# Kernel tuning notes

Measured on AMD Instinct MI355X. Metric: run time of the kernel, lower is better.

## Reference

```python
import jax, jax.numpy as jnp
import numpy as np

D_MODEL = 1024
NUM_HEADS = 16
D_K = D_MODEL // NUM_HEADS


def setup_inputs() -> dict:
    key = jax.random.key(0)
    ks = jax.random.split(key, 11)
    B, S = 4, 2048
    scale = 1.0 / np.sqrt(D_MODEL)
    inp = {
        'query': jax.random.normal(ks[0], (B, S, D_MODEL), jnp.float32),
        'key': jax.random.normal(ks[1], (B, S, D_MODEL), jnp.float32),
        'value': jax.random.normal(ks[2], (B, S, D_MODEL), jnp.float32),
        'Wq': jax.random.normal(ks[3], (D_MODEL, D_MODEL), jnp.float32) * scale,
        'bq': jnp.zeros((D_MODEL,), jnp.float32),
        'Wk': jax.random.normal(ks[4], (D_MODEL, D_MODEL), jnp.float32) * scale,
        'bk': jnp.zeros((D_MODEL,), jnp.float32),
        'Wv': jax.random.normal(ks[5], (D_MODEL, D_MODEL), jnp.float32) * scale,
        'bv': jnp.zeros((D_MODEL,), jnp.float32),
        'Wo': jax.random.normal(ks[6], (D_MODEL, D_MODEL), jnp.float32) * scale,
        'bo': jnp.zeros((D_MODEL,), jnp.float32),
    }
    return inp


def _split_heads(x):
    # [B, S, D] -> [B, H, S, d_k]
    B, S, _ = x.shape
    return x.reshape(B, S, NUM_HEADS, D_K).transpose(0, 2, 1, 3)


def reference(query, key, value, Wq, bq, Wk, bk, Wv, bv, Wo, bo):
    # torch nn.Linear: y = x @ W.T + b
    q = _split_heads(query @ Wq.T + bq)   # [B,H,Sq,dk]
    k = _split_heads(key @ Wk.T + bk)     # [B,H,Sk,dk]
    v = _split_heads(value @ Wv.T + bv)   # [B,H,Sk,dk]
    scores = jnp.einsum('bhqd,bhkd->bhqk', q, k) / jnp.sqrt(jnp.float32(D_K))
    attn = jax.nn.softmax(scores, axis=-1)
    out = jnp.einsum('bhqk,bhkd->bhqd', attn, v)  # [B,H,Sq,dk]
    B, H, Sq, dk = out.shape
    out = out.transpose(0, 2, 1, 3).reshape(B, Sq, D_MODEL)
    return out @ Wo.T + bo
```

## Files before the change

### kernel.cpp

```cpp
#include <hip/hip_runtime.h>

typedef short bf16x8 __attribute__((ext_vector_type(8)));
typedef float f32x4 __attribute__((ext_vector_type(4)));
typedef unsigned short u16;

#define S_LEN 2048
#define DM 1024
#define NH 16
#define DK 64
#define BHD ((size_t)S_LEN * DK)

#define QSCALE 0.18033688011112042f

static __device__ __forceinline__ u16 f2bf(float f) {
  union { float f; unsigned u; } x; x.f = f;
  unsigned r = x.u + 0x7FFFu + ((x.u >> 16) & 1u);
  return (u16)(r >> 16);
}

static __device__ __forceinline__ void gload_lds16(const u16* g, u16* l) {
  __builtin_amdgcn_global_load_lds(
      (const __attribute__((address_space(1))) unsigned int*)g,
      (__attribute__((address_space(3))) unsigned int*)l, 16, 0, 0);
}

__global__ __launch_bounds__(256) void conv_all(
    const float* __restrict__ q, const float* __restrict__ k, const float* __restrict__ v,
    const float* __restrict__ Wq, const float* __restrict__ Wk,
    const float* __restrict__ Wv, const float* __restrict__ Wo,
    u16* __restrict__ xq, u16* __restrict__ xk, u16* __restrict__ xv,
    u16* __restrict__ wb) {
  const int b = blockIdx.x;
  const float* s; u16* d; float sc = 1.0f; int i;
  if (b < 8192) {
    s = q; d = xq; sc = QSCALE; i = b * 256 + threadIdx.x;
  } else if (b < 16384) {
    s = k; d = xk; i = (b - 8192) * 256 + threadIdx.x;
  } else if (b < 24576) {
    s = v; d = xv; i = (b - 16384) * 256 + threadIdx.x;
  } else {
    int b2 = b - 24576, wsel = b2 >> 10;
    s = (wsel == 0) ? Wq : (wsel == 1) ? Wk : (wsel == 2) ? Wv : Wo;
    d = wb + (size_t)wsel * 1048576;
    i = (b2 & 1023) * 256 + threadIdx.x;
  }
  float4 vv = ((const float4*)s)[i];
  ushort4 h;
  h.x = f2bf(vv.x * sc); h.y = f2bf(vv.y * sc);
  h.z = f2bf(vv.z * sc); h.w = f2bf(vv.w * sc);
  ((ushort4*)d)[i] = h;
}

#define GSTAGE(DST, SRC)                                                          \
  {                                                                               \
    _Pragma("unroll") for (int j = 0; j < 4; ++j) {                               \
      gload_lds16((SRC) + (size_t)(j * 32 + (w << 3) + (l >> 3)) * 1024 +         \
                      (size_t)(((l & 7) ^ (l >> 3)) * 8),                         \
                  (DST) + (j * 256 + w * 64) * 8);                                \
    }                                                                             \
  }

__global__ __launch_bounds__(256) void proj_gemm(
    const u16* __restrict__ xq, const u16* __restrict__ xk, const u16* __restrict__ xv,
    const u16* __restrict__ wb,
    const float* __restrict__ bq, const float* __restrict__ bk, const float* __restrict__ bv,
    u16* __restrict__ qws, u16* __restrict__ kws, u16* __restrict__ vws)
{
  __shared__ u16 Al[128 * 64];
  __shared__ u16 Bl[128 * 64];
  const int z = blockIdx.z;
  const u16* Xb = (z == 0) ? xq : (z == 1) ? xk : xv;
  const u16* Wb = wb + (size_t)z * 1048576;
  const float* bias = (z == 0) ? bq : (z == 1) ? bk : bv;
  const float bscale = (z == 0) ? QSCALE : 1.0f;

  const int t = threadIdx.x;
  const int l = t & 63, w = t >> 6;
  const int lr = l & 15, lg = l >> 4;
  const int wm = w >> 1, wn = w & 1;
  const int m0 = blockIdx.x * 128, n0 = blockIdx.y * 128;
  const int sxr = lr & 7;

  f32x4 acc[4][4] = {};
  for (int k0 = 0; k0 < DM; k0 += 64) {
    __syncthreads();
    GSTAGE(Al, Xb + (size_t)m0 * 1024 + k0)
    GSTAGE(Bl, Wb + (size_t)n0 * 1024 + k0)
    __syncthreads();

    bf16x8 a[4][2], b[4][2];
#pragma unroll
    for (int mi = 0; mi < 4; ++mi) {
      const u16* rp = Al + (wm * 64 + mi * 16 + lr) * 64;
      a[mi][0] = *(const bf16x8*)(rp + ((lg ^ sxr) * 8));
      a[mi][1] = *(const bf16x8*)(rp + (((4 + lg) ^ sxr) * 8));
    }
#pragma unroll
    for (int ni = 0; ni < 4; ++ni) {
      const u16* rp = Bl + (wn * 64 + ni * 16 + lr) * 64;
      b[ni][0] = *(const bf16x8*)(rp + ((lg ^ sxr) * 8));
      b[ni][1] = *(const bf16x8*)(rp + (((4 + lg) ^ sxr) * 8));
    }
    __builtin_amdgcn_s_setprio(1);
#pragma unroll
    for (int mi = 0; mi < 4; ++mi)
#pragma unroll
      for (int ni = 0; ni < 4; ++ni) {
        acc[mi][ni] = __builtin_amdgcn_mfma_f32_16x16x32_bf16(a[mi][0], b[ni][0], acc[mi][ni], 0, 0, 0);
        acc[mi][ni] = __builtin_amdgcn_mfma_f32_16x16x32_bf16(a[mi][1], b[ni][1], acc[mi][ni], 0, 0, 0);
      }
    __builtin_amdgcn_s_setprio(0);
  }

#pragma unroll
  for (int mi = 0; mi < 4; ++mi) {
#pragma unroll
    for (int ni = 0; ni < 4; ++ni) {
#pragma unroll
      for (int r = 0; r < 4; ++r) {
        int m = m0 + wm * 64 + mi * 16 + lg * 4 + r;
        int n = n0 + wn * 64 + ni * 16 + lr;
        float y = acc[mi][ni][r] + bias[n] * bscale;
        u16 h = f2bf(y);
        int b_ = m >> 11, s = m & 2047, hh = n >> 6, d = n & 63;
        size_t head = (size_t)(b_ * NH + hh);
        if (z == 0)      qws[head * BHD + (size_t)s * DK + d] = h;
        else if (z == 1) kws[head * BHD + (size_t)s * DK + d] = h;
        else             vws[head * BHD + (size_t)d * S_LEN + s] = h;
      }
    }
  }
}

__global__ __launch_bounds__(256) void oproj_gemm(
    const u16* __restrict__ Ab, const u16* __restrict__ Wob,
    const float* __restrict__ bo, float* __restrict__ out)
{
  __shared__ u16 Al[128 * 64];
  __shared__ u16 Bl[128 * 64];
  const int t = threadIdx.x;
  const int l = t & 63, w = t >> 6;
  const int lr = l & 15, lg = l >> 4;
  const int wm = w >> 1, wn = w & 1;
  const int m0 = blockIdx.x * 128, n0 = blockIdx.y * 128;
  const int sxr = lr & 7;

  f32x4 acc[4][4] = {};
  for (int k0 = 0; k0 < DM; k0 += 64) {
    __syncthreads();
    GSTAGE(Al, Ab + (size_t)m0 * 1024 + k0)
    GSTAGE(Bl, Wob + (size_t)n0 * 1024 + k0)
    __syncthreads();

    bf16x8 a[4][2], b[4][2];
#pragma unroll
    for (int mi = 0; mi < 4; ++mi) {
      const u16* rp = Al + (wm * 64 + mi * 16 + lr) * 64;
      a[mi][0] = *(const bf16x8*)(rp + ((lg ^ sxr) * 8));
      a[mi][1] = *(const bf16x8*)(rp + (((4 + lg) ^ sxr) * 8));
    }
#pragma unroll
    for (int ni = 0; ni < 4; ++ni) {
      const u16* rp = Bl + (wn * 64 + ni * 16 + lr) * 64;
      b[ni][0] = *(const bf16x8*)(rp + ((lg ^ sxr) * 8));
      b[ni][1] = *(const bf16x8*)(rp + (((4 + lg) ^ sxr) * 8));
    }
    __builtin_amdgcn_s_setprio(1);
#pragma unroll
    for (int mi = 0; mi < 4; ++mi)
#pragma unroll
      for (int ni = 0; ni < 4; ++ni) {
        acc[mi][ni] = __builtin_amdgcn_mfma_f32_16x16x32_bf16(a[mi][0], b[ni][0], acc[mi][ni], 0, 0, 0);
        acc[mi][ni] = __builtin_amdgcn_mfma_f32_16x16x32_bf16(a[mi][1], b[ni][1], acc[mi][ni], 0, 0, 0);
      }
    __builtin_amdgcn_s_setprio(0);
  }

#pragma unroll
  for (int mi = 0; mi < 4; ++mi) {
#pragma unroll
    for (int ni = 0; ni < 4; ++ni) {
#pragma unroll
      for (int r = 0; r < 4; ++r) {
        int m = m0 + wm * 64 + mi * 16 + lg * 4 + r;
        int n = n0 + wn * 64 + ni * 16 + lr;
        out[(size_t)m * DM + n] = acc[mi][ni][r] + bo[n];
      }
    }
  }
}

__global__ __launch_bounds__(512, 8) void attn_kernel(
    const u16* __restrict__ qh, const u16* __restrict__ kh,
    const u16* __restrict__ vt, u16* __restrict__ aout)
{
  __shared__ u16 KT[2][64 * 64];
  __shared__ u16 VT[2][64 * 64];

  const int t = threadIdx.x;
  const int l = t & 63, w = t >> 6;
  const int lr = l & 15, lg = l >> 4;

  const int bid = blockIdx.x;
  const int logical = (bid & 7) * 128 + (bid >> 3);
  const int bh = logical >> 4;
  const int qb = (logical & 15) * 128 + w * 16;

  const u16* qp = qh + (size_t)bh * BHD;
  const u16* kp = kh + (size_t)bh * BHD;
  const u16* vp = vt + (size_t)bh * BHD;
  const int sx = lr & 7;

  const int srow = t >> 3;
  const int scolS = (t & 7) ^ (srow & 7);

  bf16x8 qf[2];
#pragma unroll
  for (int c = 0; c < 2; ++c)
    qf[c] = *(const bf16x8*)(qp + (size_t)(qb + lr) * DK + c * 32 + lg * 8);

  f32x4 acc[4] = {};
  float lsum = 0.0f;

#define STAGE(B, KV)                                                           \
  {                                                                            \
    gload_lds16(kp + (size_t)((KV) + srow) * DK + scolS * 8, &KT[B][w * 512]); \
    gload_lds16(vp + (size_t)srow * S_LEN + (KV) + scolS * 8, &VT[B][w * 512]);\
  }

  STAGE(0, 0)

  for (int i = 0; i < 32; ++i) {
    __syncthreads();
    if (i < 31) STAGE((i + 1) & 1, (i + 1) * 64)

    const u16* Kb = &KT[i & 1][0];
    const u16* Vb = &VT[i & 1][0];

    f32x4 sc[4] = {};
    __builtin_amdgcn_s_setprio(1);
#pragma unroll
    for (int ct = 0; ct < 4; ++ct) {
      bf16x8 k0 = *(const bf16x8*)(Kb + (ct * 16 + lr) * 64 + ((lg ^ sx) * 8));
      bf16x8 k1 = *(const bf16x8*)(Kb + (ct * 16 + lr) * 64 + (((4 + lg) ^ sx) * 8));
      sc[ct] = __builtin_amdgcn_mfma_f32_16x16x32_bf16(k0, qf[0], sc[ct], 0, 0, 0);
      sc[ct] = __builtin_amdgcn_mfma_f32_16x16x32_bf16(k1, qf[1], sc[ct], 0, 0, 0);
    }
    __builtin_amdgcn_s_setprio(0);

    unsigned cpk[4][2];
    float psum = 0.0f;
#pragma unroll
    for (int ct = 0; ct < 4; ++ct) {
      float p0 = __builtin_amdgcn_exp2f(sc[ct][0] - 8.0f);
      float p1 = __builtin_amdgcn_exp2f(sc[ct][1] - 8.0f);
      float p2 = __builtin_amdgcn_exp2f(sc[ct][2] - 8.0f);
      float p3 = __builtin_amdgcn_exp2f(sc[ct][3] - 8.0f);
      psum += (p0 + p1) + (p2 + p3);
      asm("v_cvt_pk_bf16_f32 %0, %1, %2" : "=v"(cpk[ct][0]) : "v"(p0), "v"(p1));
      asm("v_cvt_pk_bf16_f32 %0, %1, %2" : "=v"(cpk[ct][1]) : "v"(p2), "v"(p3));
    }
    lsum += psum;

    bf16x8 pf[2];
#pragma unroll
    for (int kk = 0; kk < 2; ++kk) {
      unsigned a0 = cpk[2 * kk][0], b0 = cpk[2 * kk + 1][0];
      unsigned a1 = cpk[2 * kk][1], b1 = cpk[2 * kk + 1][1];
      asm("v_permlane32_swap_b32 %0, %1" : "+v"(a0), "+v"(b0));
      asm("v_permlane16_swap_b32 %0, %1" : "+v"(a0), "+v"(b0));
      asm("v_permlane32_swap_b32 %0, %1" : "+v"(a1), "+v"(b1));
      asm("v_permlane16_swap_b32 %0, %1" : "+v"(a1), "+v"(b1));
      union { unsigned u[4]; bf16x8 v; } tmp;
      tmp.u[0] = a0; tmp.u[1] = a1; tmp.u[2] = b0; tmp.u[3] = b1;
      pf[kk] = tmp.v;
    }

    __builtin_amdgcn_s_setprio(1);
#pragma unroll
    for (int ni = 0; ni < 4; ++ni) {
      bf16x8 vf0 = *(const bf16x8*)(Vb + (ni * 16 + lr) * 64 + ((lg ^ sx) * 8));
      bf16x8 vf1 = *(const bf16x8*)(Vb + (ni * 16 + lr) * 64 + (((4 + lg) ^ sx) * 8));
      acc[ni] = __builtin_amdgcn_mfma_f32_16x16x32_bf16(pf[0], vf0, acc[ni], 0, 0, 0);
      acc[ni] = __builtin_amdgcn_mfma_f32_16x16x32_bf16(pf[1], vf1, acc[ni], 0, 0, 0);
    }
    __builtin_amdgcn_s_setprio(0);
  }
#undef STAGE

  const int b_ = bh >> 4, hh = bh & 15;
  float s_ = lsum;
  s_ += __shfl_xor(s_, 16);
  s_ += __shfl_xor(s_, 32);
  float inv = 1.0f / s_;
  float iv[4];
  iv[0] = __shfl(inv, lg * 4 + 0);
  iv[1] = __shfl(inv, lg * 4 + 1);
  iv[2] = __shfl(inv, lg * 4 + 2);
  iv[3] = __shfl(inv, lg * 4 + 3);
#pragma unroll
  for (int r = 0; r < 4; ++r) {
    int s = qb + lg * 4 + r;
#pragma unroll
    for (int ni = 0; ni < 4; ++ni)
      aout[((size_t)(b_ * S_LEN + s)) * DM + hh * DK + ni * 16 + lr] =
          f2bf(acc[ni][r] * iv[r]);
  }
}

extern "C" void kernel_launch(void* const* d_in, const int* in_sizes, int n_in,
                              void* d_out, int out_size, void* d_ws, size_t ws_size,
                              hipStream_t stream) {
  (void)in_sizes; (void)n_in; (void)out_size; (void)ws_size;
  const float* q  = (const float*)d_in[0];
  const float* k  = (const float*)d_in[1];
  const float* v  = (const float*)d_in[2];
  const float* Wq = (const float*)d_in[3];
  const float* bq = (const float*)d_in[4];
  const float* Wk = (const float*)d_in[5];
  const float* bk = (const float*)d_in[6];
  const float* Wv = (const float*)d_in[7];
  const float* bv = (const float*)d_in[8];
  const float* Wo = (const float*)d_in[9];
  const float* bo = (const float*)d_in[10];
  float* out = (float*)d_out;

  u16* qws = (u16*)d_ws;
  u16* kws = qws + (size_t)8388608;
  u16* vws = kws + (size_t)8388608;
  u16* xb  = vws + (size_t)8388608;
  u16* wb  = xb  + (size_t)8388608;
  u16* aws = xb;
  u16* kxb = (u16*)d_out;
  u16* vxb = kxb + (size_t)8388608;

  conv_all<<<dim3(28672), dim3(256), 0, stream>>>(q, k, v, Wq, Wk, Wv, Wo, xb, kxb, vxb, wb);

  proj_gemm<<<dim3(64, 8, 3), dim3(256), 0, stream>>>(xb, kxb, vxb, wb, bq, bk, bv,
                                                      qws, kws, vws);

  attn_kernel<<<dim3(1024), dim3(512), 0, stream>>>(qws, kws, vws, aws);

  oproj_gemm<<<dim3(64, 8), dim3(256), 0, stream>>>(aws, wb + 3145728, bo, out);
}
```

Baseline: 213.5 us.

## Process two 16-row query tiles per wave in attention to reuse K/V fragments

Each wave in the attention kernel now handles 32 query rows, as two 16-row MFMA tiles, instead of 16. Each K and V fragment read from LDS therefore feeds twice as many MFMAs, and each block covers 256 query rows, so the grid is halved. This cuts LDS reads and global K/V staging per unit of work. The cost is more registers per wave (launch bounds drop from 8 to 4 blocks) and half as many blocks for latency hiding.

Result: no change. 211.0 us (-1.2%).

```diff
diff --git a/kernel.cpp b/kernel.cpp
--- a/kernel.cpp
+++ b/kernel.cpp
@@ -190,7 +190,7 @@
   }
 }
 
-__global__ __launch_bounds__(512, 8) void attn_kernel(
+__global__ __launch_bounds__(512, 4) void attn_kernel(
     const u16* __restrict__ qh, const u16* __restrict__ kh,
     const u16* __restrict__ vt, u16* __restrict__ aout)
 {
@@ -202,9 +202,9 @@
   const int lr = l & 15, lg = l >> 4;
 
   const int bid = blockIdx.x;
-  const int logical = (bid & 7) * 128 + (bid >> 3);
-  const int bh = logical >> 4;
-  const int qb = (logical & 15) * 128 + w * 16;
+  const int logical = (bid & 7) * 64 + (bid >> 3);
+  const int bh = logical >> 3;
+  const int qb = (logical & 7) * 256 + w * 32;
 
   const u16* qp = qh + (size_t)bh * BHD;
   const u16* kp = kh + (size_t)bh * BHD;
@@ -214,13 +214,15 @@
   const int srow = t >> 3;
   const int scolS = (t & 7) ^ (srow & 7);
 
-  bf16x8 qf[2];
-#pragma unroll
-  for (int c = 0; c < 2; ++c)
-    qf[c] = *(const bf16x8*)(qp + (size_t)(qb + lr) * DK + c * 32 + lg * 8);
-
-  f32x4 acc[4] = {};
-  float lsum = 0.0f;
+  bf16x8 qf[2][2];
+#pragma unroll
+  for (int qi = 0; qi < 2; ++qi)
+#pragma unroll
+    for (int c = 0; c < 2; ++c)
+      qf[qi][c] = *(const bf16x8*)(qp + (size_t)(qb + qi * 16 + lr) * DK + c * 32 + lg * 8);
+
+  f32x4 acc[4][2] = {};
+  float lsum[2] = { 0.0f, 0.0f };
 
 #define STAGE(B, KV)                                                           \
   {                                                                            \
@@ -237,74 +239,86 @@
     const u16* Kb = &KT[i & 1][0];
     const u16* Vb = &VT[i & 1][0];
 
-    f32x4 sc[4] = {};
+    f32x4 sc[4][2] = {};
     __builtin_amdgcn_s_setprio(1);
 #pragma unroll
     for (int ct = 0; ct < 4; ++ct) {
       bf16x8 k0 = *(const bf16x8*)(Kb + (ct * 16 + lr) * 64 + ((lg ^ sx) * 8));
       bf16x8 k1 = *(const bf16x8*)(Kb + (ct * 16 + lr) * 64 + (((4 + lg) ^ sx) * 8));
-      sc[ct] = __builtin_amdgcn_mfma_f32_16x16x32_bf16(k0, qf[0], sc[ct], 0, 0, 0);
-      sc[ct] = __builtin_amdgcn_mfma_f32_16x16x32_bf16(k1, qf[1], sc[ct], 0, 0, 0);
+      sc[ct][0] = __builtin_amdgcn_mfma_f32_16x16x32_bf16(k0, qf[0][0], sc[ct][0], 0, 0, 0);
+      sc[ct][0] = __builtin_amdgcn_mfma_f32_16x16x32_bf16(k1, qf[0][1], sc[ct][0], 0, 0, 0);
+      sc[ct][1] = __builtin_amdgcn_mfma_f32_16x16x32_bf16(k0, qf[1][0], sc[ct][1], 0, 0, 0);
+      sc[ct][1] = __builtin_amdgcn_mfma_f32_16x16x32_bf16(k1, qf[1][1], sc[ct][1], 0, 0, 0);
     }
     __builtin_amdgcn_s_setprio(0);
 
-    unsigned cpk[4][2];
-    float psum = 0.0f;
-#pragma unroll
-    for (int ct = 0; ct < 4; ++ct) {
-      float p0 = __builtin_amdgcn_exp2f(sc[ct][0] - 8.0f);
-      float p1 = __builtin_amdgcn_exp2f(sc[ct][1] - 8.0f);
-      float p2 = __builtin_amdgcn_exp2f(sc[ct][2] - 8.0f);
-      float p3 = __builtin_amdgcn_exp2f(sc[ct][3] - 8.0f);
-      psum += (p0 + p1) + (p2 + p3);
-      asm("v_cvt_pk_bf16_f32 %0, %1, %2" : "=v"(cpk[ct][0]) : "v"(p0), "v"(p1));
-      asm("v_cvt_pk_bf16_f32 %0, %1, %2" : "=v"(cpk[ct][1]) : "v"(p2), "v"(p3));
-    }
-    lsum += psum;
-
-    bf16x8 pf[2];
-#pragma unroll
-    for (int kk = 0; kk < 2; ++kk) {
-      unsigned a0 = cpk[2 * kk][0], b0 = cpk[2 * kk + 1][0];
-      unsigned a1 = cpk[2 * kk][1], b1 = cpk[2 * kk + 1][1];
-      asm("v_permlane32_swap_b32 %0, %1" : "+v"(a0), "+v"(b0));
-      asm("v_permlane16_swap_b32 %0, %1" : "+v"(a0), "+v"(b0));
-      asm("v_permlane32_swap_b32 %0, %1" : "+v"(a1), "+v"(b1));
-      asm("v_permlane16_swap_b32 %0, %1" : "+v"(a1), "+v"(b1));
-      union { unsigned u[4]; bf16x8 v; } tmp;
-      tmp.u[0] = a0; tmp.u[1] = a1; tmp.u[2] = b0; tmp.u[3] = b1;
-      pf[kk] = tmp.v;
-    }
+    unsigned cpk[2][4][2];
+#pragma unroll
+    for (int qi = 0; qi < 2; ++qi) {
+      float psum = 0.0f;
+#pragma unroll
+      for (int ct = 0; ct < 4; ++ct) {
+        float p0 = __builtin_amdgcn_exp2f(sc[ct][qi][0] - 8.0f);
+        float p1 = __builtin_amdgcn_exp2f(sc[ct][qi][1] - 8.0f);
+        float p2 = __builtin_amdgcn_exp2f(sc[ct][qi][2] - 8.0f);
+        float p3 = __builtin_amdgcn_exp2f(sc[ct][qi][3] - 8.0f);
+        psum += (p0 + p1) + (p2 + p3);
+        asm("v_cvt_pk_bf16_f32 %0, %1, %2" : "=v"(cpk[qi][ct][0]) : "v"(p0), "v"(p1));
+        asm("v_cvt_pk_bf16_f32 %0, %1, %2" : "=v"(cpk[qi][ct][1]) : "v"(p2), "v"(p3));
+      }
+      lsum[qi] += psum;
+    }
+
+    bf16x8 pf[2][2];
+#pragma unroll
+    for (int qi = 0; qi < 2; ++qi)
+#pragma unroll
+      for (int kk = 0; kk < 2; ++kk) {
+        unsigned a0 = cpk[qi][2 * kk][0], b0 = cpk[qi][2 * kk + 1][0];
+        unsigned a1 = cpk[qi][2 * kk][1], b1 = cpk[qi][2 * kk + 1][1];
+        asm("v_permlane32_swap_b32 %0, %1" : "+v"(a0), "+v"(b0));
+        asm("v_permlane16_swap_b32 %0, %1" : "+v"(a0), "+v"(b0));
+        asm("v_permlane32_swap_b32 %0, %1" : "+v"(a1), "+v"(b1));
+        asm("v_permlane16_swap_b32 %0, %1" : "+v"(a1), "+v"(b1));
+        union { unsigned u[4]; bf16x8 v; } tmp;
+        tmp.u[0] = a0; tmp.u[1] = a1; tmp.u[2] = b0; tmp.u[3] = b1;
+        pf[qi][kk] = tmp.v;
+      }
 
     __builtin_amdgcn_s_setprio(1);
 #pragma unroll
     for (int ni = 0; ni < 4; ++ni) {
       bf16x8 vf0 = *(const bf16x8*)(Vb + (ni * 16 + lr) * 64 + ((lg ^ sx) * 8));
       bf16x8 vf1 = *(const bf16x8*)(Vb + (ni * 16 + lr) * 64 + (((4 + lg) ^ sx) * 8));
-      acc[ni] = __builtin_amdgcn_mfma_f32_16x16x32_bf16(pf[0], vf0, acc[ni], 0, 0, 0);
-      acc[ni] = __builtin_amdgcn_mfma_f32_16x16x32_bf16(pf[1], vf1, acc[ni], 0, 0, 0);
+      acc[ni][0] = __builtin_amdgcn_mfma_f32_16x16x32_bf16(pf[0][0], vf0, acc[ni][0], 0, 0, 0);
+      acc[ni][0] = __builtin_amdgcn_mfma_f32_16x16x32_bf16(pf[0][1], vf1, acc[ni][0], 0, 0, 0);
+      acc[ni][1] = __builtin_amdgcn_mfma_f32_16x16x32_bf16(pf[1][0], vf0, acc[ni][1], 0, 0, 0);
+      acc[ni][1] = __builtin_amdgcn_mfma_f32_16x16x32_bf16(pf[1][1], vf1, acc[ni][1], 0, 0, 0);
     }
     __builtin_amdgcn_s_setprio(0);
   }
 #undef STAGE
 
   const int b_ = bh >> 4, hh = bh & 15;
-  float s_ = lsum;
-  s_ += __shfl_xor(s_, 16);
-  s_ += __shfl_xor(s_, 32);
-  float inv = 1.0f / s_;
-  float iv[4];
-  iv[0] = __shfl(inv, lg * 4 + 0);
-  iv[1] = __shfl(inv, lg * 4 + 1);
-  iv[2] = __shfl(inv, lg * 4 + 2);
-  iv[3] = __shfl(inv, lg * 4 + 3);
-#pragma unroll
-  for (int r = 0; r < 4; ++r) {
-    int s = qb + lg * 4 + r;
-#pragma unroll
-    for (int ni = 0; ni < 4; ++ni)
-      aout[((size_t)(b_ * S_LEN + s)) * DM + hh * DK + ni * 16 + lr] =
-          f2bf(acc[ni][r] * iv[r]);
+#pragma unroll
+  for (int qi = 0; qi < 2; ++qi) {
+    float s_ = lsum[qi];
+    s_ += __shfl_xor(s_, 16);
+    s_ += __shfl_xor(s_, 32);
+    float inv = 1.0f / s_;
+    float iv[4];
+    iv[0] = __shfl(inv, lg * 4 + 0);
+    iv[1] = __shfl(inv, lg * 4 + 1);
+    iv[2] = __shfl(inv, lg * 4 + 2);
+    iv[3] = __shfl(inv, lg * 4 + 3);
+#pragma unroll
+    for (int r = 0; r < 4; ++r) {
+      int s = qb + qi * 16 + lg * 4 + r;
+#pragma unroll
+      for (int ni = 0; ni < 4; ++ni)
+        aout[((size_t)(b_ * S_LEN + s)) * DM + hh * DK + ni * 16 + lr] =
+            f2bf(acc[ni][qi][r] * iv[r]);
+    }
   }
 }
 
@@ -339,7 +353,7 @@
   proj_gemm<<<dim3(64, 8, 3), dim3(256), 0, stream>>>(xb, kxb, vxb, wb, bq, bk, bv,
                                                       qws, kws, vws);
 
-  attn_kernel<<<dim3(1024), dim3(512), 0, stream>>>(qws, kws, vws, aws);
+  attn_kernel<<<dim3(512), dim3(512), 0, stream>>>(qws, kws, vws, aws);
 
   oproj_gemm<<<dim3(64, 8), dim3(256), 0, stream>>>(aws, wb + 3145728, bo, out);
 }
```
